# Kernel tuning notes

Measured on AMD Instinct MI355X. Metric: run time of the kernel, lower is better.

## Reference

```python
import jax, jax.numpy as jnp
import numpy as np

N, E, DIM, H = 100000, 1600000, 128, 8
HD = DIM // H


def setup_inputs() -> dict:
    key = jax.random.key(0)
    ks = jax.random.split(key, 12)
    inp = {
        'x': jax.random.normal(ks[0], (N, DIM), dtype=jnp.float32),
        'src': jax.random.randint(ks[1], (E,), 0, N, dtype=jnp.int32),
        'dst': jax.random.randint(ks[2], (E,), 0, N, dtype=jnp.int32),
    }
    scale = 1.0 / np.sqrt(DIM)
    for i, nm in enumerate(['q', 'k', 'v', 'o']):
        inp['W' + nm] = jax.random.normal(ks[3 + 2 * i], (DIM, DIM), dtype=jnp.float32) * scale
        inp['b' + nm] = jax.random.normal(ks[4 + 2 * i], (DIM,), dtype=jnp.float32) * 0.01
    return inp


def reference(x, src, dst, Wq, bq, Wk, bk, Wv, bv, Wo, bo):
    n = x.shape[0]
    q = (x @ Wq + bq).reshape(n, H, HD)
    k = (x @ Wk + bk).reshape(n, H, HD)
    v = (x @ Wv + bv).reshape(n, H, HD)
    # per-edge score: dot(q[src], k[dst]) over head_dim  -> [E, H]
    scores = jnp.einsum('ehd,ehd->eh', q[src], k[dst]) / np.sqrt(HD).astype(np.float32)
    # edge softmax grouped by destination node
    m = jax.ops.segment_max(scores, dst, num_segments=n)        # [N, H]
    e = jnp.exp(scores - m[dst])                                 # [E, H]
    z = jax.ops.segment_sum(e, dst, num_segments=n)              # [N, H]
    attn = e / z[dst]                                            # [E, H]
    # weighted scatter-sum of source values into destinations
    agg = jax.ops.segment_sum(v[src] * attn[:, :, None], dst, num_segments=n)  # [N, H, HD]
    out = agg.reshape(n, DIM) @ Wo + bo
    return out
```

## Files before the change

### kernel.cpp

```cpp
#include <hip/hip_runtime.h>
#include <hip/hip_bf16.h>
#include <math.h>


#define CAP 64
#define CUR_STRIDE 16
#define BCHUNK 4096

typedef __attribute__((ext_vector_type(8))) short short8;
typedef __attribute__((ext_vector_type(4))) float f32x4;

__device__ inline unsigned short f2bf(float f) {
    unsigned u = __float_as_uint(f);
    unsigned r = u + 0x7fffu + ((u >> 16) & 1u);
    return (unsigned short)(r >> 16);
}
__device__ inline float bfhi2f(unsigned u) { return __uint_as_float(u & 0xffff0000u); }
__device__ inline float bflo2f(unsigned u) { return __uint_as_float(u << 16); }

__device__ inline float w_perm(const float* Wq, const float* Wk, const float* Wv,
                               int k, int c) {
    if (c < 256) {
        int hh = c >> 4, r = c & 15;
        return (r < 8) ? Wq[k * 128 + hh * 8 + r] : Wv[k * 128 + hh * 8 + (r - 8)];
    }
    return Wk[k * 128 + (c - 256)];
}

__global__ void pack_b_kernel(const float* __restrict__ Wq, const float* __restrict__ Wk,
                              const float* __restrict__ Wv, const float* __restrict__ Wo,
                              const float* __restrict__ bq, const float* __restrict__ bk,
                              const float* __restrict__ bv,
                              short* __restrict__ BqkvP, short* __restrict__ BoP,
                              float* __restrict__ bqkv) {
    int t = blockIdx.x * 256 + threadIdx.x;
    if (t < 24 * 4 * 64 * 8) {
        int j = t & 7, l = (t >> 3) & 63, ks = (t >> 9) & 3, ct = t >> 11;
        int c = ct * 16 + (l & 15);
        int k = ks * 32 + (l >> 4) * 8 + j;
        BqkvP[t] = (short)f2bf(w_perm(Wq, Wk, Wv, k, c));
    }
    if (t < 8 * 4 * 64 * 8) {
        int j = t & 7, l = (t >> 3) & 63, ks = (t >> 9) & 3, ct = t >> 11;
        int c = ct * 16 + (l & 15);
        int k = ks * 32 + (l >> 4) * 8 + j;
        BoP[t] = (short)f2bf(Wo[k * 128 + c]);
    }
    if (t < 384) {
        float v;
        if (t < 256) {
            int hh = t >> 4, r = t & 15;
            v = (r < 8) ? bq[hh * 8 + r] : bv[hh * 8 + (r - 8)];
        } else v = bk[t - 256];
        bqkv[t] = v;
    }
}

#define QKV_STRIDE 392
__global__ __launch_bounds__(256) void gemm_qkv_mfma(const float* __restrict__ A,
        const short* __restrict__ Bp, const float* __restrict__ bias,
        short* __restrict__ qv, short* __restrict__ kb, int M) {
    __shared__ short stage[4][16][QKV_STRIDE];
    int w = threadIdx.x >> 6, l = threadIdx.x & 63;
    int row0 = blockIdx.x * 64 + w * 16;
    int lr = l & 15, lk = l >> 4;

    f32x4 acc[24];
    #pragma unroll
    for (int ct = 0; ct < 24; ++ct) {
        float b = bias[ct * 16 + lr];
        acc[ct][0] = b; acc[ct][1] = b; acc[ct][2] = b; acc[ct][3] = b;
    }

    int arow = row0 + lr;
    bool rowok = arow < M;
    const float* arp = A + (size_t)arow * 128;

    #pragma unroll
    for (int ks = 0; ks < 4; ++ks) {
        f32x4 a0 = {0.f, 0.f, 0.f, 0.f}, a1 = {0.f, 0.f, 0.f, 0.f};
        if (rowok) {
            a0 = *(const f32x4*)(arp + ks * 32 + lk * 8);
            a1 = *(const f32x4*)(arp + ks * 32 + lk * 8 + 4);
        }
        short8 af;
        af[0] = (short)f2bf(a0[0]); af[1] = (short)f2bf(a0[1]);
        af[2] = (short)f2bf(a0[2]); af[3] = (short)f2bf(a0[3]);
        af[4] = (short)f2bf(a1[0]); af[5] = (short)f2bf(a1[1]);
        af[6] = (short)f2bf(a1[2]); af[7] = (short)f2bf(a1[3]);
        #pragma unroll
        for (int ct = 0; ct < 24; ++ct) {
            short8 bf = *(const short8*)(Bp + ((size_t)(ct * 4 + ks) * 64 + l) * 8);
            acc[ct] = __builtin_amdgcn_mfma_f32_16x16x32_bf16(af, bf, acc[ct], 0, 0, 0);
        }
    }

    #pragma unroll
    for (int ct = 0; ct < 24; ++ct) {
        int c = ct * 16 + lr;
        #pragma unroll
        for (int j = 0; j < 4; ++j)
            stage[w][lk * 4 + j][c] = (short)f2bf(acc[ct][j]);
    }
    __syncthreads();

    #pragma unroll
    for (int it = 0; it < 8; ++it) {
        int rr = it * 2 + (l >> 5);
        int row = row0 + rr;
        if (row < M) {
            short8 vqv = *(const short8*)&stage[w][rr][(l & 31) * 8];
            *(short8*)(qv + (size_t)row * 256 + (l & 31) * 8) = vqv;
        }
    }
    #pragma unroll
    for (int it = 0; it < 4; ++it) {
        int rr = it * 4 + (l >> 4);
        int row = row0 + rr;
        if (row < M) {
            short8 vk = *(const short8*)&stage[w][rr][256 + (l & 15) * 8];
            *(short8*)(kb + (size_t)row * 128 + (l & 15) * 8) = vk;
        }
    }
}

__global__ __launch_bounds__(256) void build_kernel(const int* __restrict__ src,
        const int* __restrict__ dst, int* __restrict__ cursor, int* __restrict__ csr,
        int E, int per8) {
    int xcd = blockIdx.x & 7;
    int chunk = blockIdx.x >> 3;
    int lo = xcd * per8, hi = lo + per8;
    int base = chunk * BCHUNK;
    #pragma unroll
    for (int it = 0; it < BCHUNK / 256; ++it) {
        int e = base + it * 256 + threadIdx.x;
        if (e < E) {
            int d = __builtin_nontemporal_load(dst + e);
            if (d >= lo && d < hi) {
                int s = __builtin_nontemporal_load(src + e);
                int slot = atomicAdd(&cursor[d << 4], 1);
                if (slot < CAP) csr[((size_t)d << 6) + slot] = s;
            }
        }
    }
}

#define AGG_STRIDE 68

#define EDGE_ITER(EIDX)                                                        \
    {                                                                          \
        int eidx = (EIDX);                                                     \
        bool act = eidx < n;                                                   \
        int s = act ? ep[eidx] : 0;                                            \
        const uint4* qp = (const uint4*)(qv + (size_t)s * 256 + h2 * 16);      \
        uint4 qq = qp[0];                                                      \
        uint4 vv = qp[1];                                                      \
        float p = bflo2f(qq.x) * kf[0] + bfhi2f(qq.x) * kf[1]                  \
                + bflo2f(qq.y) * kf[2] + bfhi2f(qq.y) * kf[3]                  \
                + bflo2f(qq.z) * kf[4] + bfhi2f(qq.z) * kf[5]                  \
                + bflo2f(qq.w) * kf[6] + bfhi2f(qq.w) * kf[7];                 \
        p += __shfl_xor(p, 1);                                                 \
        float ee = act ? __expf(p * 0.25f) : 0.f;                              \
        z += ee;                                                               \
        ag[0] += ee * bflo2f(vv.x); ag[1] += ee * bfhi2f(vv.x);                \
        ag[2] += ee * bflo2f(vv.y); ag[3] += ee * bfhi2f(vv.y);                \
        ag[4] += ee * bflo2f(vv.z); ag[5] += ee * bfhi2f(vv.z);                \
        ag[6] += ee * bflo2f(vv.w); ag[7] += ee * bfhi2f(vv.w);                \
    }

__global__ __launch_bounds__(256) void edge_out_kernel(const short* __restrict__ qv,
        const short* __restrict__ kb, const int* __restrict__ cursor,
        const int* __restrict__ csr, const short* __restrict__ BoP,
        const float* __restrict__ bo, float* __restrict__ out, int N, int per8) {
    __shared__ unsigned aggLds[16][AGG_STRIDE];
    int w  = threadIdx.x >> 6;
    int l  = threadIdx.x & 63;
    int lr = l & 15, lk = l >> 4;
    int h2 = l & 15;
    int slot = l >> 4;
    int xcd = blockIdx.x & 7;
    int jb  = blockIdx.x >> 3;
    int sliceN = per8 < (N - xcd * per8) ? per8 : (N - xcd * per8);
    int local0 = jb * 16;

    #pragma unroll
    for (int q = 0; q < 4; ++q) {
        int i = w * 4 + q;
        int local = local0 + i;
        if (local < sliceN) {
            int d = xcd * per8 + local;
            int deg = cursor[d << 4];
            int n = (deg < CAP) ? deg : CAP;
            const int* ep = csr + ((size_t)d << 6);

            uint4 kk = *(const uint4*)(kb + (size_t)d * 128 + h2 * 8);
            float kf[8];
            kf[0] = bflo2f(kk.x); kf[1] = bfhi2f(kk.x);
            kf[2] = bflo2f(kk.y); kf[3] = bfhi2f(kk.y);
            kf[4] = bflo2f(kk.z); kf[5] = bfhi2f(kk.z);
            kf[6] = bflo2f(kk.w); kf[7] = bfhi2f(kk.w);

            float z = 0.f;
            float ag[8] = {0.f, 0.f, 0.f, 0.f, 0.f, 0.f, 0.f, 0.f};

            int base = 0;
            for (; base + 8 <= n + 7; base += 8) {
                EDGE_ITER(base + slot)
                EDGE_ITER(base + 4 + slot)
                if (base + 8 >= n) break;
            }

            z += __shfl_xor(z, 16);
            z += __shfl_xor(z, 32);
            #pragma unroll
            for (int j = 0; j < 8; ++j) {
                ag[j] += __shfl_xor(ag[j], 16);
                ag[j] += __shfl_xor(ag[j], 32);
            }

            float zi = (z > 0.f) ? 1.0f / z : 0.f;
            if (slot == 0) {
                #pragma unroll
                for (int j = 0; j < 4; ++j) {
                    unsigned pk = (unsigned)f2bf(ag[2 * j] * zi) |
                                  ((unsigned)f2bf(ag[2 * j + 1] * zi) << 16);
                    aggLds[i][h2 * 4 + j] = pk;
                }
            }
        }
    }
    __syncthreads();

    f32x4 acc[2];
    #pragma unroll
    for (int t = 0; t < 2; ++t) {
        float b = bo[(w * 2 + t) * 16 + lr];
        acc[t][0] = b; acc[t][1] = b; acc[t][2] = b; acc[t][3] = b;
    }

    #pragma unroll
    for (int ks = 0; ks < 4; ++ks) {
        short8 af = *(const short8*)&aggLds[lr][ks * 16 + lk * 4];
        #pragma unroll
        for (int t = 0; t < 2; ++t) {
            int ct = w * 2 + t;
            short8 bf = *(const short8*)(BoP + ((size_t)(ct * 4 + ks) * 64 + l) * 8);
            acc[t] = __builtin_amdgcn_mfma_f32_16x16x32_bf16(af, bf, acc[t], 0, 0, 0);
        }
    }

    #pragma unroll
    for (int t = 0; t < 2; ++t) {
        int c = (w * 2 + t) * 16 + lr;
        #pragma unroll
        for (int j = 0; j < 4; ++j) {
            int localr = local0 + lk * 4 + j;
            if (localr < sliceN) {
                int r = xcd * per8 + localr;
                out[(size_t)r * 128 + c] = acc[t][j];
            }
        }
    }
}

extern "C" void kernel_launch(void* const* d_in, const int* in_sizes, int n_in,
                              void* d_out, int out_size, void* d_ws, size_t ws_size,
                              hipStream_t stream) {
    const float* x   = (const float*)d_in[0];
    const int*   src = (const int*)d_in[1];
    const int*   dst = (const int*)d_in[2];
    const float* Wq  = (const float*)d_in[3];
    const float* bq  = (const float*)d_in[4];
    const float* Wk  = (const float*)d_in[5];
    const float* bk  = (const float*)d_in[6];
    const float* Wv  = (const float*)d_in[7];
    const float* bv  = (const float*)d_in[8];
    const float* Wo  = (const float*)d_in[9];
    const float* bo  = (const float*)d_in[10];
    float* out = (float*)d_out;

    int N = in_sizes[0] / 128;
    int E = in_sizes[1];
    int per8 = (N + 7) / 8;

    char* ws = (char*)d_ws;
    size_t off = 0;
    auto alloc = [&](size_t bytes) -> void* {
        void* p = ws + off;
        off = (off + bytes + 255) & ~(size_t)255;
        return p;
    };
    short* BqkvP  = (short*)alloc((size_t)24 * 4 * 64 * 8 * 2);
    short* BoP    = (short*)alloc((size_t)8 * 4 * 64 * 8 * 2);
    float* bqkv   = (float*)alloc(384 * 4);
    short* qv     = (short*)alloc((size_t)N * 256 * 2);
    short* kb     = (short*)alloc((size_t)N * 128 * 2);
    int* csr      = (int*)alloc((size_t)N * CAP * 4);
    int* cursor   = (int*)alloc((size_t)N * CUR_STRIDE * 4);
    (void)ws_size; (void)n_in; (void)out_size;

    hipMemsetAsync(cursor, 0, (size_t)N * CUR_STRIDE * 4, stream);

    pack_b_kernel<<<192, 256, 0, stream>>>(Wq, Wk, Wv, Wo, bq, bk, bv, BqkvP, BoP, bqkv);

    gemm_qkv_mfma<<<(N + 63) / 64, 256, 0, stream>>>(x, BqkvP, bqkv, qv, kb, N);

    int nchunks = (E + BCHUNK - 1) / BCHUNK;
    build_kernel<<<nchunks * 8, 256, 0, stream>>>(src, dst, cursor, csr, E, per8);

    int nb16 = (per8 + 15) / 16;
    edge_out_kernel<<<nb16 * 8, 256, 0, stream>>>(qv, kb, cursor, csr, BoP, bo, out, N, per8);
}
```

Before: 298.4 us.

## Pack cursor densely, vectorize CSR index loads, drop nontemporal loads

Removes the 16-int padding on the per-node atomic cursor so the counter array and its memset shrink 16x. This trades less memset and cache footprint for more atomic contention on shared cache lines. The edge loop now loads four neighbor indices per lane with one int4 load and processes 16 edges per iteration instead of 8, with per-edge activity masks. The src/dst loads in the build kernel switch from nontemporal to normal loads, so the repeated scans across the 8 XCD passes may hit in cache.

Result: faster. 276.6 us (-7.3%).

```diff
diff --git a/kernel.cpp b/kernel.cpp
--- a/kernel.cpp
+++ b/kernel.cpp
@@ -4,7 +4,6 @@
 
 
 #define CAP 64
-#define CUR_STRIDE 16
 #define BCHUNK 4096
 
 typedef __attribute__((ext_vector_type(8))) short short8;
@@ -135,10 +134,10 @@
     for (int it = 0; it < BCHUNK / 256; ++it) {
         int e = base + it * 256 + threadIdx.x;
         if (e < E) {
-            int d = __builtin_nontemporal_load(dst + e);
+            int d = dst[e];
             if (d >= lo && d < hi) {
-                int s = __builtin_nontemporal_load(src + e);
-                int slot = atomicAdd(&cursor[d << 4], 1);
+                int s = src[e];
+                int slot = atomicAdd(&cursor[d], 1);
                 if (slot < CAP) csr[((size_t)d << 6) + slot] = s;
             }
         }
@@ -147,11 +146,10 @@
 
 #define AGG_STRIDE 68
 
-#define EDGE_ITER(EIDX)                                                        \
+#define EDGE_ITER(EI, ACT)                                                     \
     {                                                                          \
-        int eidx = (EIDX);                                                     \
-        bool act = eidx < n;                                                   \
-        int s = act ? ep[eidx] : 0;                                            \
+        bool act = (ACT);                                                      \
+        int s = act ? (EI) : 0;                                                \
         const uint4* qp = (const uint4*)(qv + (size_t)s * 256 + h2 * 16);      \
         uint4 qq = qp[0];                                                      \
         uint4 vv = qp[1];                                                      \
@@ -189,7 +187,7 @@
         int local = local0 + i;
         if (local < sliceN) {
             int d = xcd * per8 + local;
-            int deg = cursor[d << 4];
+            int deg = cursor[d];
             int n = (deg < CAP) ? deg : CAP;
             const int* ep = csr + ((size_t)d << 6);
 
@@ -203,11 +201,13 @@
             float z = 0.f;
             float ag[8] = {0.f, 0.f, 0.f, 0.f, 0.f, 0.f, 0.f, 0.f};
 
-            int base = 0;
-            for (; base + 8 <= n + 7; base += 8) {
-                EDGE_ITER(base + slot)
-                EDGE_ITER(base + 4 + slot)
-                if (base + 8 >= n) break;
+            for (int b0 = 0; b0 < n; b0 += 16) {
+                int bb = b0 + slot * 4;
+                int4 e4 = *(const int4*)(ep + bb);
+                EDGE_ITER(e4.x, bb + 0 < n)
+                EDGE_ITER(e4.y, bb + 1 < n)
+                EDGE_ITER(e4.z, bb + 2 < n)
+                EDGE_ITER(e4.w, bb + 3 < n)
             }
 
             z += __shfl_xor(z, 16);
@@ -296,10 +296,10 @@
     short* qv     = (short*)alloc((size_t)N * 256 * 2);
     short* kb     = (short*)alloc((size_t)N * 128 * 2);
     int* csr      = (int*)alloc((size_t)N * CAP * 4);
-    int* cursor   = (int*)alloc((size_t)N * CUR_STRIDE * 4);
+    int* cursor   = (int*)alloc((size_t)N * 4);
     (void)ws_size; (void)n_in; (void)out_size;
 
-    hipMemsetAsync(cursor, 0, (size_t)N * CUR_STRIDE * 4, stream);
+    hipMemsetAsync(cursor, 0, (size_t)N * 4, stream);
 
     pack_b_kernel<<<192, 256, 0, stream>>>(Wq, Wk, Wv, Wo, bq, bk, bv, BqkvP, BoP, bqkv);
 
```
